# Kernel optimization log

Hardware: AMD Instinct MI355X
Metric: run time of the kernel (lower is better)

Reference implementation:

```python
import jax, jax.numpy as jnp
import numpy as np

N_WORDS = 30000
EMB_DIM = 784  # 28*28
MAT_DIM = 28
BATCH = 1024
SEQ_LEN = 64


def setup_inputs() -> dict:
    key = jax.random.key(0)
    k_sent, k_tab = jax.random.split(key)
    # token ids in [0, n_words]; row 0 is the neutral (identity) / padding element
    sent = jax.random.randint(k_sent, (BATCH, SEQ_LEN), 0, N_WORDS + 1, dtype=jnp.int32).astype(jnp.int64)
    eye_flat = jnp.eye(MAT_DIM, dtype=jnp.float32).reshape(-1)
    # 'identity' init strategy: identity + small gaussian noise (scale kept small for stability of long products)
    table = eye_flat + 0.01 * jax.random.normal(k_tab, (N_WORDS + 1, EMB_DIM), dtype=jnp.float32)
    table = table.at[0].set(eye_flat)  # neutral element at padding_idx=0
    return {"sent": sent, "table": table}


def reference(sent, table):
    # sent: [B, S] int ids; table: [n_words+1, d*d]
    B, S = sent.shape
    d = MAT_DIM
    word_mats = table[sent].reshape(B, S, d, d)  # embedding lookup + unflatten
    # CMOW: continual multiplication cur = cur @ W_i, sequential over seq dim
    init = word_mats[:, 0]                      # [B, d, d]
    rest = jnp.moveaxis(word_mats[:, 1:], 1, 0)  # [S-1, B, d, d]

    def step(cur, w):
        return jnp.matmul(cur, w), None

    cur, _ = jax.lax.scan(step, init, rest)
    return cur.reshape(B, d * d)  # flatten matrix back to embedding
```

## Files before the change

kernel.cpp:

```cpp
#include <hip/hip_runtime.h>
#include <stdint.h>

#define SEQ 64
#define D 28
#define EMB 784
#define NW 4
#define CH 16
#define BUFF 832
#define SCRW 36

typedef float float4v __attribute__((ext_vector_type(4)));
typedef __bf16 bf16x8 __attribute__((ext_vector_type(8)));

union FragU { unsigned u[4]; bf16x8 v; };

__device__ __forceinline__ unsigned fbits(float x) { union { float f; unsigned u; } t; t.f = x; return t.u; }
__device__ __forceinline__ float fof(unsigned u) { union { unsigned u; float f; } t; t.u = u; return t.f; }

__device__ __forceinline__ void split_frags(const float x[8], bf16x8& hi, bf16x8& lo)
{
    FragU H, L;
#pragma unroll
    for (int p = 0; p < 4; ++p) {
        unsigned ua = fbits(x[2 * p]), ub = fbits(x[2 * p + 1]);
        H.u[p] = (ua >> 16) | (ub & 0xFFFF0000u);
        unsigned la = fbits(x[2 * p]     - fof(ua & 0xFFFF0000u));
        unsigned lb = fbits(x[2 * p + 1] - fof(ub & 0xFFFF0000u));
        L.u[p] = (la >> 16) | (lb & 0xFFFF0000u);
    }
    hi = H.v; lo = L.v;
}

struct AB { bf16x8 h, l; };

__device__ __forceinline__ AB make_frag4(const float y[4])
{
    float x[8] = { y[0], y[1], y[2], y[3], 0.f, 0.f, 0.f, 0.f };
    AB r; split_frags(x, r.h, r.l); return r;
}

__device__ __forceinline__ void dma_row(const float* grow, float* lbuf, int lane)
{
    const char* g16 = (const char*)grow + lane * 16;
    const char* g4  = (const char*)grow + 3072 + lane * 4;
    char* l = (char*)lbuf;
    __builtin_amdgcn_global_load_lds((const __attribute__((address_space(1))) void*)(g16),
                                     (__attribute__((address_space(3))) void*)(l), 16, 0, 0);
    __builtin_amdgcn_global_load_lds((const __attribute__((address_space(1))) void*)(g16 + 1024),
                                     (__attribute__((address_space(3))) void*)(l + 1024), 16, 0, 0);
    __builtin_amdgcn_global_load_lds((const __attribute__((address_space(1))) void*)(g16 + 2048),
                                     (__attribute__((address_space(3))) void*)(l + 2048), 16, 0, 0);
    __builtin_amdgcn_global_load_lds((const __attribute__((address_space(1))) void*)(g4),
                                     (__attribute__((address_space(3))) void*)(l + 3072), 4, 0, 0);
}

__device__ __forceinline__ void stepT(const float* mat, int stride,
                                      float4v acc[2][2], int lane)
{
    const int c = lane & 15;
    const int quad = lane >> 4;
    const bool q3 = (quad == 3);

    float av[2][2][4];
#pragma unroll
    for (int KB = 0; KB < 2; ++KB)
#pragma unroll
        for (int t = 0; t < 4; ++t) {
            int k = 16 * KB + 4 * quad + t;
            if (k > 27) k = 27;
#pragma unroll
            for (int Ro = 0; Ro < 2; ++Ro)
                av[Ro][KB][t] = mat[k * stride + 16 * Ro + c];
        }

    AB Bf[2][2];
#pragma unroll
    for (int KB = 0; KB < 2; ++KB)
#pragma unroll
        for (int Co = 0; Co < 2; ++Co) {
            float y[4] = { acc[KB][Co][0], acc[KB][Co][1], acc[KB][Co][2], acc[KB][Co][3] };
            Bf[KB][Co] = make_frag4(y);
        }

    AB Af[2][2];
#pragma unroll
    for (int Ro = 0; Ro < 2; ++Ro)
#pragma unroll
        for (int KB = 0; KB < 2; ++KB) {
            float y[4] = { av[Ro][KB][0], av[Ro][KB][1], av[Ro][KB][2], av[Ro][KB][3] };
            if (q3 && KB == 1) { y[0] = y[1] = y[2] = y[3] = 0.f; }
            Af[Ro][KB] = make_frag4(y);
        }

#pragma unroll
    for (int Ro = 0; Ro < 2; ++Ro)
#pragma unroll
        for (int Co = 0; Co < 2; ++Co) {
            float4v d = {0.f, 0.f, 0.f, 0.f};
#pragma unroll
            for (int KB = 0; KB < 2; ++KB) {
                d = __builtin_amdgcn_mfma_f32_16x16x32_bf16(Af[Ro][KB].h, Bf[KB][Co].h, d, 0, 0, 0);
                d = __builtin_amdgcn_mfma_f32_16x16x32_bf16(Af[Ro][KB].h, Bf[KB][Co].l, d, 0, 0, 0);
                d = __builtin_amdgcn_mfma_f32_16x16x32_bf16(Af[Ro][KB].l, Bf[KB][Co].h, d, 0, 0, 0);
            }
            acc[Ro][Co] = d;
        }
}

template <int CNT, typename F>
__device__ __forceinline__ void chainT(F rowptr, float* B0, float* B1,
                                       float4v acc[2][2], int lane)
{
    const int c = lane & 15;
    const int quad = lane >> 4;

    dma_row(rowptr(0), B0, lane);
    dma_row(rowptr(1), B1, lane);
    __builtin_amdgcn_s_waitcnt(0x0074);

#pragma unroll
    for (int R = 0; R < 2; ++R)
#pragma unroll
        for (int Cc = 0; Cc < 2; ++Cc) {
            int rcl = 16 * Cc + c; if (rcl > 27) rcl = 27;
            acc[R][Cc] = *(const float4v*)&B0[rcl * D + 16 * R + 4 * quad];
        }
    __builtin_amdgcn_s_waitcnt(0xC07F);

#pragma unroll 1
    for (int j = 1; j < CNT; ++j) {
        const int jn = (j + 1 < CNT) ? (j + 1) : j;
        float* nB = (j & 1) ? B0 : B1;
        float* cB = (j & 1) ? B1 : B0;
        dma_row(rowptr(jn), nB, lane);

        __builtin_amdgcn_sched_barrier(0);
        __builtin_amdgcn_s_waitcnt(0x0074);
        __builtin_amdgcn_sched_barrier(0);

        stepT(cB, D, acc, lane);
    }
}

__global__ __launch_bounds__(NW * 64, 1) void w2m_fusedT(
    const int* __restrict__ sent,
    const float* __restrict__ table,
    float* __restrict__ out)
{
    __shared__ float SH[NW * 2 * BUFF] __attribute__((aligned(16)));
    const int lane = threadIdx.x & 63;
    const int wid  = threadIdx.x >> 6;
    const int b = blockIdx.x;

    float* B0 = &SH[wid * 2 * BUFF];
    float* B1 = B0 + BUFF;

    const int myidx = sent[b * SEQ + CH * wid + (lane & (CH - 1))];
    int jl[CH];
#pragma unroll
    for (int j = 0; j < CH; ++j) jl[j] = __builtin_amdgcn_readlane(myidx, j);

    float4v acc[2][2];
    chainT<CH>([&](int j) { return table + (size_t)jl[j] * EMB; },
               B0, B1, acc, lane);

    const int c = lane & 15;
    const int quad = lane >> 4;

    __builtin_amdgcn_s_waitcnt(0x0070);
    __builtin_amdgcn_sched_barrier(0);
    float* SCR = &SH[wid * 2 * BUFF];
#pragma unroll
    for (int R = 0; R < 2; ++R)
#pragma unroll
        for (int Cc = 0; Cc < 2; ++Cc)
#pragma unroll
            for (int i = 0; i < 4; ++i)
                SCR[(16 * R + 4 * quad + i) * SCRW + 16 * Cc + c] = acc[R][Cc][i];
    __syncthreads();

    const float* S3 = &SH[3 * 2 * BUFF];
#pragma unroll
    for (int R = 0; R < 2; ++R)
#pragma unroll
        for (int Cc = 0; Cc < 2; ++Cc)
            acc[R][Cc] = *(const float4v*)&S3[(16 * Cc + c) * SCRW + 16 * R + 4 * quad];

#pragma unroll 1
    for (int j = 2; j >= 0; --j)
        stepT(&SH[j * 2 * BUFF], SCRW, acc, lane);

    if (wid == 0) {
        float* orow = out + (size_t)b * EMB;
#pragma unroll
        for (int R = 0; R < 2; ++R)
#pragma unroll
            for (int Cc = 0; Cc < 2; ++Cc)
#pragma unroll
                for (int i = 0; i < 4; ++i) {
                    const int row = 16 * R + 4 * quad + i;
                    const int col = 16 * Cc + c;
                    if (row < D && col < D) orow[row * D + col] = acc[R][Cc][i];
                }
    }
}

extern "C" void kernel_launch(void* const* d_in, const int* in_sizes, int n_in,
                              void* d_out, int out_size, void* d_ws, size_t ws_size,
                              hipStream_t stream) {
    const int* sent = (const int*)d_in[0];
    const float* table = (const float*)d_in[1];
    float* out = (float*)d_out;
    const int batch = in_sizes[0] / SEQ;
    (void)d_ws; (void)ws_size;

    hipLaunchKernelGGL(w2m_fusedT, dim3(batch), dim3(NW * 64), 0, stream,
                       sent, table, out);
}
```

Baseline: 159.8 us.

## Triple-buffer table row prefetch and pack split-bf16 products into two MFMAs

Replaces the double-buffered row DMA with a three-deep buffer so each step prefetches two rows ahead. The sequence loop is fully unrolled with precomputed per-lane LDS pointers and a compile-time stride. The hi/lo bf16 split is repacked so the three MFMAs per k-block (hh, hl, lh) fit into two, by putting A's hi and lo in one fragment against duplicated B-hi and a B-lo fragment padded with zeros. The launch-bounds hint is raised to 4 blocks per CU. In exchange it uses more LDS per block, grows code size through the unroll, and makes the accumulation order more intricate.

After: 153.3 us. 1.04x faster.

```diff
diff --git a/kernel.cpp b/kernel.cpp
--- a/kernel.cpp
+++ b/kernel.cpp
@@ -17,26 +17,19 @@
 __device__ __forceinline__ unsigned fbits(float x) { union { float f; unsigned u; } t; t.f = x; return t.u; }
 __device__ __forceinline__ float fof(unsigned u) { union { unsigned u; float f; } t; t.u = u; return t.f; }
 
-__device__ __forceinline__ void split_frags(const float x[8], bf16x8& hi, bf16x8& lo)
-{
-    FragU H, L;
-#pragma unroll
-    for (int p = 0; p < 4; ++p) {
-        unsigned ua = fbits(x[2 * p]), ub = fbits(x[2 * p + 1]);
-        H.u[p] = (ua >> 16) | (ub & 0xFFFF0000u);
-        unsigned la = fbits(x[2 * p]     - fof(ua & 0xFFFF0000u));
-        unsigned lb = fbits(x[2 * p + 1] - fof(ub & 0xFFFF0000u));
-        L.u[p] = (la >> 16) | (lb & 0xFFFF0000u);
-    }
-    hi = H.v; lo = L.v;
-}
-
-struct AB { bf16x8 h, l; };
-
-__device__ __forceinline__ AB make_frag4(const float y[4])
-{
-    float x[8] = { y[0], y[1], y[2], y[3], 0.f, 0.f, 0.f, 0.f };
-    AB r; split_frags(x, r.h, r.l); return r;
+struct HL4 { unsigned h01, h23, l01, l23; };
+__device__ __forceinline__ HL4 hilo4(float x0, float x1, float x2, float x3) {
+    unsigned u0 = fbits(x0), u1 = fbits(x1), u2 = fbits(x2), u3 = fbits(x3);
+    HL4 r;
+    r.h01 = (u0 >> 16) | (u1 & 0xFFFF0000u);
+    r.h23 = (u2 >> 16) | (u3 & 0xFFFF0000u);
+    unsigned l0 = fbits(x0 - fof(u0 & 0xFFFF0000u));
+    unsigned l1 = fbits(x1 - fof(u1 & 0xFFFF0000u));
+    unsigned l2 = fbits(x2 - fof(u2 & 0xFFFF0000u));
+    unsigned l3 = fbits(x3 - fof(u3 & 0xFFFF0000u));
+    r.l01 = (l0 >> 16) | (l1 & 0xFFFF0000u);
+    r.l23 = (l2 >> 16) | (l3 & 0xFFFF0000u);
+    return r;
 }
 
 __device__ __forceinline__ void dma_row(const float* grow, float* lbuf, int lane)
@@ -54,42 +47,44 @@
                                      (__attribute__((address_space(3))) void*)(l + 3072), 4, 0, 0);
 }
 
-__device__ __forceinline__ void stepT(const float* mat, int stride,
-                                      float4v acc[2][2], int lane)
+template<int STRIDE>
+__device__ __forceinline__ void stepT(const float* a0, const float* a1,
+                                      float4v acc[2][2], bool q3)
 {
-    const int c = lane & 15;
-    const int quad = lane >> 4;
-    const bool q3 = (quad == 3);
-
     float av[2][2][4];
 #pragma unroll
+    for (int t = 0; t < 4; ++t)
+#pragma unroll
+        for (int Ro = 0; Ro < 2; ++Ro) {
+            av[Ro][0][t] = a0[t * STRIDE + 16 * Ro];
+            av[Ro][1][t] = a1[t * STRIDE + 16 * Ro];
+        }
+#pragma unroll
+    for (int Ro = 0; Ro < 2; ++Ro)
+#pragma unroll
+        for (int t = 0; t < 4; ++t)
+            av[Ro][1][t] = q3 ? 0.f : av[Ro][1][t];
+
+    FragU Af[2][2];
+#pragma unroll
+    for (int Ro = 0; Ro < 2; ++Ro)
+#pragma unroll
+        for (int KB = 0; KB < 2; ++KB) {
+            HL4 h = hilo4(av[Ro][KB][0], av[Ro][KB][1], av[Ro][KB][2], av[Ro][KB][3]);
+            Af[Ro][KB].u[0] = h.h01; Af[Ro][KB].u[1] = h.h23;
+            Af[Ro][KB].u[2] = h.l01; Af[Ro][KB].u[3] = h.l23;
+        }
+
+    FragU Bd[2][2], B2[2][2];
+#pragma unroll
     for (int KB = 0; KB < 2; ++KB)
 #pragma unroll
-        for (int t = 0; t < 4; ++t) {
-            int k = 16 * KB + 4 * quad + t;
-            if (k > 27) k = 27;
-#pragma unroll
-            for (int Ro = 0; Ro < 2; ++Ro)
-                av[Ro][KB][t] = mat[k * stride + 16 * Ro + c];
-        }
-
-    AB Bf[2][2];
-#pragma unroll
-    for (int KB = 0; KB < 2; ++KB)
-#pragma unroll
         for (int Co = 0; Co < 2; ++Co) {
-            float y[4] = { acc[KB][Co][0], acc[KB][Co][1], acc[KB][Co][2], acc[KB][Co][3] };
-            Bf[KB][Co] = make_frag4(y);
-        }
-
-    AB Af[2][2];
-#pragma unroll
-    for (int Ro = 0; Ro < 2; ++Ro)
-#pragma unroll
-        for (int KB = 0; KB < 2; ++KB) {
-            float y[4] = { av[Ro][KB][0], av[Ro][KB][1], av[Ro][KB][2], av[Ro][KB][3] };
-            if (q3 && KB == 1) { y[0] = y[1] = y[2] = y[3] = 0.f; }
-            Af[Ro][KB] = make_frag4(y);
+            HL4 h = hilo4(acc[KB][Co][0], acc[KB][Co][1], acc[KB][Co][2], acc[KB][Co][3]);
+            Bd[KB][Co].u[0] = h.h01; Bd[KB][Co].u[1] = h.h23;
+            Bd[KB][Co].u[2] = h.h01; Bd[KB][Co].u[3] = h.h23;
+            B2[KB][Co].u[0] = h.l01; B2[KB][Co].u[1] = h.l23;
+            B2[KB][Co].u[2] = 0u;    B2[KB][Co].u[3] = 0u;
         }
 
 #pragma unroll
@@ -99,77 +94,78 @@
             float4v d = {0.f, 0.f, 0.f, 0.f};
 #pragma unroll
             for (int KB = 0; KB < 2; ++KB) {
-                d = __builtin_amdgcn_mfma_f32_16x16x32_bf16(Af[Ro][KB].h, Bf[KB][Co].h, d, 0, 0, 0);
-                d = __builtin_amdgcn_mfma_f32_16x16x32_bf16(Af[Ro][KB].h, Bf[KB][Co].l, d, 0, 0, 0);
-                d = __builtin_amdgcn_mfma_f32_16x16x32_bf16(Af[Ro][KB].l, Bf[KB][Co].h, d, 0, 0, 0);
+                d = __builtin_amdgcn_mfma_f32_16x16x32_bf16(Af[Ro][KB].v, Bd[KB][Co].v, d, 0, 0, 0);
+                d = __builtin_amdgcn_mfma_f32_16x16x32_bf16(Af[Ro][KB].v, B2[KB][Co].v, d, 0, 0, 0);
             }
             acc[Ro][Co] = d;
         }
 }
 
-template <int CNT, typename F>
-__device__ __forceinline__ void chainT(F rowptr, float* B0, float* B1,
-                                       float4v acc[2][2], int lane)
-{
-    const int c = lane & 15;
-    const int quad = lane >> 4;
-
-    dma_row(rowptr(0), B0, lane);
-    dma_row(rowptr(1), B1, lane);
-    __builtin_amdgcn_s_waitcnt(0x0074);
-
-#pragma unroll
-    for (int R = 0; R < 2; ++R)
-#pragma unroll
-        for (int Cc = 0; Cc < 2; ++Cc) {
-            int rcl = 16 * Cc + c; if (rcl > 27) rcl = 27;
-            acc[R][Cc] = *(const float4v*)&B0[rcl * D + 16 * R + 4 * quad];
-        }
-    __builtin_amdgcn_s_waitcnt(0xC07F);
-
-#pragma unroll 1
-    for (int j = 1; j < CNT; ++j) {
-        const int jn = (j + 1 < CNT) ? (j + 1) : j;
-        float* nB = (j & 1) ? B0 : B1;
-        float* cB = (j & 1) ? B1 : B0;
-        dma_row(rowptr(jn), nB, lane);
-
-        __builtin_amdgcn_sched_barrier(0);
-        __builtin_amdgcn_s_waitcnt(0x0074);
-        __builtin_amdgcn_sched_barrier(0);
-
-        stepT(cB, D, acc, lane);
-    }
-}
-
-__global__ __launch_bounds__(NW * 64, 1) void w2m_fusedT(
+__global__ __launch_bounds__(NW * 64, 4) void w2m_fusedT3(
     const int* __restrict__ sent,
     const float* __restrict__ table,
     float* __restrict__ out)
 {
-    __shared__ float SH[NW * 2 * BUFF] __attribute__((aligned(16)));
+    __shared__ float SH[NW * 3 * BUFF] __attribute__((aligned(16)));
     const int lane = threadIdx.x & 63;
     const int wid  = threadIdx.x >> 6;
     const int b = blockIdx.x;
-
-    float* B0 = &SH[wid * 2 * BUFF];
+    const int c = lane & 15;
+    const int quad = lane >> 4;
+    const bool q3 = (quad == 3);
+    const int qc = q3 ? 2 : quad;
+
+    float* B0 = &SH[wid * 3 * BUFF];
     float* B1 = B0 + BUFF;
+    float* B2b = B0 + 2 * BUFF;
 
     const int myidx = sent[b * SEQ + CH * wid + (lane & (CH - 1))];
     int jl[CH];
 #pragma unroll
     for (int j = 0; j < CH; ++j) jl[j] = __builtin_amdgcn_readlane(myidx, j);
 
+    dma_row(table + (size_t)jl[0] * EMB, B0, lane);
+    dma_row(table + (size_t)jl[1] * EMB, B1, lane);
+    dma_row(table + (size_t)jl[2] * EMB, B2b, lane);
+    __builtin_amdgcn_s_waitcnt(0x0078);
+
     float4v acc[2][2];
-    chainT<CH>([&](int j) { return table + (size_t)jl[j] * EMB; },
-               B0, B1, acc, lane);
-
-    const int c = lane & 15;
-    const int quad = lane >> 4;
+#pragma unroll
+    for (int R = 0; R < 2; ++R)
+#pragma unroll
+        for (int Cc = 0; Cc < 2; ++Cc) {
+            int rcl = 16 * Cc + c; if (rcl > 27) rcl = 27;
+            acc[R][Cc] = *(const float4v*)&B0[rcl * D + 16 * R + 4 * quad];
+        }
+
+    const float* a00 = B0  + 4 * quad * D + c;
+    const float* a10 = B0  + (16 + 4 * qc) * D + c;
+    const float* a01 = B1  + 4 * quad * D + c;
+    const float* a11 = B1  + (16 + 4 * qc) * D + c;
+    const float* a02 = B2b + 4 * quad * D + c;
+    const float* a12 = B2b + (16 + 4 * qc) * D + c;
+
+#pragma unroll
+    for (int j = 1; j < CH; ++j) {
+        __builtin_amdgcn_s_waitcnt(0xC07F);
+        const int jn = (j + 2 < CH) ? j + 2 : CH - 1;
+        const int tb = (j + 2) % 3;
+        float* nB = (tb == 0) ? B0 : (tb == 1) ? B1 : B2b;
+        dma_row(table + (size_t)jl[jn] * EMB, nB, lane);
+
+        __builtin_amdgcn_sched_barrier(0);
+        __builtin_amdgcn_s_waitcnt(0x0078);
+        __builtin_amdgcn_sched_barrier(0);
+
+        const int cb = j % 3;
+        if (cb == 0)      stepT<D>(a00, a10, acc, q3);
+        else if (cb == 1) stepT<D>(a01, a11, acc, q3);
+        else              stepT<D>(a02, a12, acc, q3);
+    }
 
     __builtin_amdgcn_s_waitcnt(0x0070);
     __builtin_amdgcn_sched_barrier(0);
-    float* SCR = &SH[wid * 2 * BUFF];
+    float* SCR = B0;
 #pragma unroll
     for (int R = 0; R < 2; ++R)
 #pragma unroll
@@ -179,16 +175,19 @@
                 SCR[(16 * R + 4 * quad + i) * SCRW + 16 * Cc + c] = acc[R][Cc][i];
     __syncthreads();
 
-    const float* S3 = &SH[3 * 2 * BUFF];
+    const float* S3 = &SH[3 * 3 * BUFF];
 #pragma unroll
     for (int R = 0; R < 2; ++R)
 #pragma unroll
         for (int Cc = 0; Cc < 2; ++Cc)
             acc[R][Cc] = *(const float4v*)&S3[(16 * Cc + c) * SCRW + 16 * R + 4 * quad];
 
-#pragma unroll 1
-    for (int j = 2; j >= 0; --j)
-        stepT(&SH[j * 2 * BUFF], SCRW, acc, lane);
+#pragma unroll
+    for (int j = 2; j >= 0; --j) {
+        const float* reg = &SH[j * 3 * BUFF];
+        stepT<SCRW>(reg + 4 * quad * SCRW + c,
+                    reg + (16 + 4 * quad) * SCRW + c, acc, q3);
+    }
 
     if (wid == 0) {
         float* orow = out + (size_t)b * EMB;
@@ -214,6 +213,6 @@
     const int batch = in_sizes[0] / SEQ;
     (void)d_ws; (void)ws_size;
 
-    hipLaunchKernelGGL(w2m_fusedT, dim3(batch), dim3(NW * 64), 0, stream,
+    hipLaunchKernelGGL(w2m_fusedT3, dim3(batch), dim3(NW * 64), 0, stream,
                        sent, table, out);
 }
```
